# Kernel optimization log

Measured on AMD Instinct MI355X. Metric: run time of the kernel, lower is better.

Reference implementation:

```python
import jax, jax.numpy as jnp
import numpy as np


def setup_inputs() -> dict:
    key = jax.random.key(0)
    k = jax.random.split(key, 6)
    B = 65536
    x = jax.random.normal(k[0], (B, 784), dtype=jnp.float32)
    conv_w = jax.random.normal(k[1], (3, 3), dtype=jnp.float32)
    # torch Linear: weight [out,in], bias [out]; uniform(-1/sqrt(in),1/sqrt(in)) init approximated
    fc1_w = jax.random.uniform(k[2], (128, 26 * 26), dtype=jnp.float32, minval=-1, maxval=1) / jnp.sqrt(676.0)
    fc1_b = jax.random.uniform(k[3], (128,), dtype=jnp.float32, minval=-1, maxval=1) / jnp.sqrt(676.0)
    fc2_w = jax.random.uniform(k[4], (10, 128), dtype=jnp.float32, minval=-1, maxval=1) / jnp.sqrt(128.0)
    fc2_b = jax.random.uniform(k[5], (10,), dtype=jnp.float32, minval=-1, maxval=1) / jnp.sqrt(128.0)
    return {"x": x, "conv_w": conv_w, "fc1_w": fc1_w, "fc1_b": fc1_b, "fc2_w": fc2_w, "fc2_b": fc2_b}


def _forward(x, conv_w, fc1_w, fc1_b, fc2_w, fc2_b):
    B = x.shape[0]
    img = x.reshape(B, 1, 28, 28)  # NCHW, single channel
    kern = conv_w.reshape(1, 1, 3, 3)  # OIHW
    # valid 3x3 cross-correlation -> (B,1,26,26), same math as the nested-loop Convolve
    conv = jax.lax.conv_general_dilated(
        img, kern, window_strides=(1, 1), padding="VALID",
        dimension_numbers=("NCHW", "OIHW", "NCHW"))
    h = conv.reshape(B, 26 * 26)
    h = jax.nn.relu(h @ fc1_w.T + fc1_b)
    return h @ fc2_w.T + fc2_b  # (B,10)


def reference(x, conv_w, fc1_w, fc1_b, fc2_w, fc2_b):
    return _forward(x, conv_w, fc1_w, fc1_b, fc2_w, fc2_b)
```

## Files before the change

### kernel.cpp

```cpp
#include <hip/hip_runtime.h>
#include <hip/hip_bf16.h>

typedef float  f32x4  __attribute__((ext_vector_type(4)));
typedef short  short8 __attribute__((ext_vector_type(8)));

#define NKT 25
#define BM  128
#define AB  8192
#define BB  8192
#define BOFF (3 * AB)
#define POOLB (3 * AB + 4 * BB)

static __device__ __forceinline__ unsigned short f2bf(float f) {
    unsigned int u = __float_as_uint(f);
    unsigned int r = (u + 0x7fffu + ((u >> 16) & 1u)) >> 16;
    return (unsigned short)r;
}
static __device__ __forceinline__ float bf2f(unsigned short h) {
    return __uint_as_float(((unsigned int)h) << 16);
}
static __device__ __forceinline__ uint2 pack4(f32x4 v) {
    __hip_bfloat162 p0 = __float22bfloat162_rn(make_float2(v[0], v[1]));
    __hip_bfloat162 p1 = __float22bfloat162_rn(make_float2(v[2], v[3]));
    uint2 r;
    r.x = *reinterpret_cast<unsigned int*>(&p0);
    r.y = *reinterpret_cast<unsigned int*>(&p1);
    return r;
}

__global__ __launch_bounds__(256) void weff_prep(
    const float* __restrict__ fc1_w,
    const float* __restrict__ conv_w,
    unsigned short* __restrict__ weff4)
{
    int idx = blockIdx.x * 256 + threadIdx.x;
    if (idx >= 128 * 800) return;
    int o = idx / 800, p = idx - o * 800;
    float s = 0.f;
    if (p < 784) {
        int y = p / 28, xx = p - y * 28;
        #pragma unroll
        for (int dr = 0; dr < 3; ++dr) {
            int r = y - dr;
            if (r < 0 || r > 25) continue;
            #pragma unroll
            for (int dc = 0; dc < 3; ++dc) {
                int c = xx - dc;
                if (c < 0 || c > 25) continue;
                s += fc1_w[o * 676 + r * 26 + c] * conv_w[dr * 3 + dc];
            }
        }
    }
    int kt = p >> 5, kk = p & 31;
    weff4[kt * 4096 + (kk >> 3) * 1024 + o * 8 + (kk & 7)] = f2bf(s);
}

__global__ __launch_bounds__(512, 4) void fused_fwd(
    const float* __restrict__ x,
    const unsigned short* __restrict__ weff4,
    const float* __restrict__ fc1_b,
    const float* __restrict__ fc2_w,
    const float* __restrict__ fc2_b,
    float* __restrict__ out,
    int B)
{
    __shared__ __align__(16) char pool[POOLB];
    __shared__ float fc2w_s[1280];
    __shared__ float fc2b_s[16];

    const int tid  = threadIdx.x;
    const int lane = tid & 63;
    const int wid  = tid >> 6;
    const int wr   = wid >> 1;
    const int wc   = wid & 1;
    const int r16  = lane & 15;
    const int kc   = lane >> 4;
    const int m0   = blockIdx.x * BM;

    for (int i = tid; i < 1280; i += 512) fc2w_s[i] = fc2_w[i];
    if (tid < 10) fc2b_s[tid] = fc2_b[tid];
    asm volatile("s_waitcnt vmcnt(0)" ::: "memory");

    const int sr   = tid >> 3;
    const int g    = tid & 7;
    const int k2w  = g >> 1, half = g & 1;
    int row0 = m0 + sr;      if (row0 >= B) row0 = B - 1;
    int row1 = m0 + sr + 64; if (row1 >= B) row1 = B - 1;
    const float* xr0 = x + (size_t)row0 * 784;
    const float* xr1 = x + (size_t)row1 * 784;
    const int awb = k2w * 2048 + sr * 16 + half * 8;

    f32x4 av[3][2];

#define LD_A(s_, kt_) do {                                                    \
        int k_ = (kt_) * 32 + g * 4; if (k_ > 780) k_ = 0;                    \
        av[s_][0] = *reinterpret_cast<const f32x4*>(xr0 + k_);                \
        av[s_][1] = *reinterpret_cast<const f32x4*>(xr1 + k_);                \
    } while (0)

#define WR_A(s_, bi_) do {                                                    \
        uint2 q0_ = pack4(av[s_][0]);                                         \
        uint2 q1_ = pack4(av[s_][1]);                                         \
        char* ba_ = pool + (bi_) * AB + awb;                                  \
        *reinterpret_cast<uint2*>(ba_)        = q0_;                          \
        *reinterpret_cast<uint2*>(ba_ + 1024) = q1_;                          \
    } while (0)

#define GL_B(bi_, kt_) __builtin_amdgcn_global_load_lds(                      \
        (const __attribute__((address_space(1))) void*)                      \
            (weff4 + (size_t)(kt_) * 4096 + tid * 8),                         \
        (__attribute__((address_space(3))) void*)                            \
            (pool + BOFF + (bi_) * BB + tid * 16), 16, 0, 0)

    const int aoff = kc * 2048 + (wr * 32 + r16) * 16;
    const int boff = BOFF + kc * 2048 + (wc * 64 + r16) * 16;

    f32x4 acc[2][4];
    #pragma unroll
    for (int m = 0; m < 2; ++m)
        #pragma unroll
        for (int j = 0; j < 4; ++j) acc[m][j] = (f32x4)(0.f);

    LD_A(0, 0);
    GL_B(0, 0); GL_B(1, 1); GL_B(2, 2);
    LD_A(1, 1); LD_A(2, 2);
    WR_A(0, 0);

    #pragma unroll
    for (int i = 0; i < NKT; ++i) {
        asm volatile("s_waitcnt vmcnt(6) lgkmcnt(0)" ::: "memory");
        __builtin_amdgcn_s_barrier();
        __builtin_amdgcn_sched_barrier(0);

        const char* pa = pool + (i % 3) * AB;
        const char* pb = pool + (i % 4) * BB;
        short8 a0 = *reinterpret_cast<const short8*>(pa + aoff);
        short8 a1 = *reinterpret_cast<const short8*>(pa + aoff + 256);
        short8 b0 = *reinterpret_cast<const short8*>(pb + boff);
        short8 b1 = *reinterpret_cast<const short8*>(pb + boff + 256);
        short8 b2 = *reinterpret_cast<const short8*>(pb + boff + 512);
        short8 b3 = *reinterpret_cast<const short8*>(pb + boff + 768);

        const int kn = (i + 3 <= 24) ? (i + 3) : 24;
        LD_A((i + 3) % 3, kn);
        GL_B((i + 3) % 4, kn);
        WR_A((i + 1) % 3, (i + 1) % 3);

        acc[0][0] = __builtin_amdgcn_mfma_f32_16x16x32_bf16(a0, b0, acc[0][0], 0, 0, 0);
        acc[0][1] = __builtin_amdgcn_mfma_f32_16x16x32_bf16(a0, b1, acc[0][1], 0, 0, 0);
        acc[0][2] = __builtin_amdgcn_mfma_f32_16x16x32_bf16(a0, b2, acc[0][2], 0, 0, 0);
        acc[0][3] = __builtin_amdgcn_mfma_f32_16x16x32_bf16(a0, b3, acc[0][3], 0, 0, 0);
        acc[1][0] = __builtin_amdgcn_mfma_f32_16x16x32_bf16(a1, b0, acc[1][0], 0, 0, 0);
        acc[1][1] = __builtin_amdgcn_mfma_f32_16x16x32_bf16(a1, b1, acc[1][1], 0, 0, 0);
        acc[1][2] = __builtin_amdgcn_mfma_f32_16x16x32_bf16(a1, b2, acc[1][2], 0, 0, 0);
        acc[1][3] = __builtin_amdgcn_mfma_f32_16x16x32_bf16(a1, b3, acc[1][3], 0, 0, 0);
    }
#undef LD_A
#undef WR_A
#undef GL_B

    asm volatile("s_waitcnt vmcnt(0) lgkmcnt(0)" ::: "memory");
    __builtin_amdgcn_s_barrier();
    __builtin_amdgcn_sched_barrier(0);

    unsigned short (*Hs)[136] = (unsigned short (*)[136])pool;
    #pragma unroll
    for (int m = 0; m < 2; ++m) {
        #pragma unroll
        for (int j = 0; j < 4; ++j) {
            int ncol = wc * 64 + j * 16 + r16;
            float bias = fc1_b[ncol];
            #pragma unroll
            for (int r = 0; r < 4; ++r) {
                int mrow = wr * 32 + m * 16 + kc * 4 + r;
                float h = acc[m][j][r] + bias;
                Hs[mrow][ncol] = f2bf(h > 0.f ? h : 0.f);
            }
        }
    }
    __syncthreads();

    #pragma unroll
    for (int it = 0; it < 3; ++it) {
        int idx = it * 512 + tid;
        if (idx < BM * 10) {
            int row = idx / 10, j = idx - row * 10;
            if ((m0 + row) < B) {
                float sum = fc2b_s[j];
                const float* wrow = &fc2w_s[j * 128];
                #pragma unroll
                for (int n8 = 0; n8 < 16; ++n8) {
                    short8 h = *reinterpret_cast<const short8*>(&Hs[row][n8 * 8]);
                    #pragma unroll
                    for (int k2 = 0; k2 < 8; ++k2)
                        sum += bf2f(((unsigned short*)&h)[k2]) * wrow[n8 * 8 + k2];
                }
                out[(size_t)(m0 + row) * 10 + j] = sum;
            }
        }
    }
}

extern "C" void kernel_launch(void* const* d_in, const int* in_sizes, int n_in,
                              void* d_out, int out_size, void* d_ws, size_t ws_size,
                              hipStream_t stream) {
    const float* x      = (const float*)d_in[0];
    const float* conv_w = (const float*)d_in[1];
    const float* fc1_w  = (const float*)d_in[2];
    const float* fc1_b  = (const float*)d_in[3];
    const float* fc2_w  = (const float*)d_in[4];
    const float* fc2_b  = (const float*)d_in[5];
    float* out = (float*)d_out;
    unsigned short* weff4 = (unsigned short*)d_ws;

    int B = in_sizes[0] / 784;

    weff_prep<<<(128 * 800 + 255) / 256, 256, 0, stream>>>(fc1_w, conv_w, weff4);

    int nblk = (B + BM - 1) / BM;
    fused_fwd<<<nblk, 512, 0, stream>>>(x, weff4, fc1_b, fc2_w, fc2_b, out, B);
}
```

Measured before the change: 59.74 us.

## Halve row tile to 64, shrink LDS ring, move fc2 weights to bf16 global

Cuts the per-block M tile from 128 to 64 rows. Each wave now issues four MFMAs per k-step instead of eight, and the LDS B ring drops from four stages to three, so the launch bound rises to 8 blocks per CU. fc2 weights are converted to bf16 once in the prep kernel and read from global/L1 instead of being staged into LDS, which frees shared memory. The aim is higher occupancy to hide streaming latency on the x reads. In exchange, the weff B tiles are reloaded twice as often per row, and fc2 weights lose precision.

```diff
diff --git a/kernel.cpp b/kernel.cpp
--- a/kernel.cpp
+++ b/kernel.cpp
@@ -4,12 +4,12 @@
 typedef float  f32x4  __attribute__((ext_vector_type(4)));
 typedef short  short8 __attribute__((ext_vector_type(8)));
 
-#define NKT 25
-#define BM  128
-#define AB  8192
-#define BB  8192
-#define BOFF (3 * AB)
-#define POOLB (3 * AB + 4 * BB)
+#define NKT   25
+#define BM    64
+#define AB    4096
+#define BB    8192
+#define BOFFS (3 * AB)
+#define POOLB (3 * AB + 3 * BB)
 
 static __device__ __forceinline__ unsigned short f2bf(float f) {
     unsigned int u = __float_as_uint(f);
@@ -31,10 +31,12 @@
 __global__ __launch_bounds__(256) void weff_prep(
     const float* __restrict__ fc1_w,
     const float* __restrict__ conv_w,
-    unsigned short* __restrict__ weff4)
+    const float* __restrict__ fc2_w,
+    unsigned short* __restrict__ ws)
 {
     int idx = blockIdx.x * 256 + threadIdx.x;
     if (idx >= 128 * 800) return;
+    if (idx < 1280) ws[102400 + idx] = f2bf(fc2_w[idx]);
     int o = idx / 800, p = idx - o * 800;
     float s = 0.f;
     if (p < 784) {
@@ -52,21 +54,18 @@
         }
     }
     int kt = p >> 5, kk = p & 31;
-    weff4[kt * 4096 + (kk >> 3) * 1024 + o * 8 + (kk & 7)] = f2bf(s);
-}
-
-__global__ __launch_bounds__(512, 4) void fused_fwd(
+    ws[kt * 4096 + (kk >> 3) * 1024 + o * 8 + (kk & 7)] = f2bf(s);
+}
+
+__global__ __launch_bounds__(512, 8) void fused_fwd(
     const float* __restrict__ x,
     const unsigned short* __restrict__ weff4,
     const float* __restrict__ fc1_b,
-    const float* __restrict__ fc2_w,
     const float* __restrict__ fc2_b,
     float* __restrict__ out,
     int B)
 {
     __shared__ __align__(16) char pool[POOLB];
-    __shared__ float fc2w_s[1280];
-    __shared__ float fc2b_s[16];
 
     const int tid  = threadIdx.x;
     const int lane = tid & 63;
@@ -76,84 +75,69 @@
     const int r16  = lane & 15;
     const int kc   = lane >> 4;
     const int m0   = blockIdx.x * BM;
-
-    for (int i = tid; i < 1280; i += 512) fc2w_s[i] = fc2_w[i];
-    if (tid < 10) fc2b_s[tid] = fc2_b[tid];
-    asm volatile("s_waitcnt vmcnt(0)" ::: "memory");
-
-    const int sr   = tid >> 3;
-    const int g    = tid & 7;
-    const int k2w  = g >> 1, half = g & 1;
-    int row0 = m0 + sr;      if (row0 >= B) row0 = B - 1;
-    int row1 = m0 + sr + 64; if (row1 >= B) row1 = B - 1;
-    const float* xr0 = x + (size_t)row0 * 784;
-    const float* xr1 = x + (size_t)row1 * 784;
-    const int awb = k2w * 2048 + sr * 16 + half * 8;
-
-    f32x4 av[3][2];
+    const unsigned short* fc2wb = weff4 + 102400;
+
+    const int sr = tid >> 3;
+    const int g  = tid & 7;
+    int grow = m0 + sr; if (grow >= B) grow = B - 1;
+    const float* xr = x + (size_t)grow * 784;
+    const int awb = (g >> 1) * 1024 + sr * 16 + (g & 1) * 8;
+
+    f32x4 av[4];
 
 #define LD_A(s_, kt_) do {                                                    \
         int k_ = (kt_) * 32 + g * 4; if (k_ > 780) k_ = 0;                    \
-        av[s_][0] = *reinterpret_cast<const f32x4*>(xr0 + k_);                \
-        av[s_][1] = *reinterpret_cast<const f32x4*>(xr1 + k_);                \
+        av[s_] = *reinterpret_cast<const f32x4*>(xr + k_);                    \
     } while (0)
 
 #define WR_A(s_, bi_) do {                                                    \
-        uint2 q0_ = pack4(av[s_][0]);                                         \
-        uint2 q1_ = pack4(av[s_][1]);                                         \
-        char* ba_ = pool + (bi_) * AB + awb;                                  \
-        *reinterpret_cast<uint2*>(ba_)        = q0_;                          \
-        *reinterpret_cast<uint2*>(ba_ + 1024) = q1_;                          \
+        uint2 q_ = pack4(av[s_]);                                             \
+        *reinterpret_cast<uint2*>(pool + (bi_) * AB + awb) = q_;              \
     } while (0)
 
 #define GL_B(bi_, kt_) __builtin_amdgcn_global_load_lds(                      \
         (const __attribute__((address_space(1))) void*)                      \
             (weff4 + (size_t)(kt_) * 4096 + tid * 8),                         \
         (__attribute__((address_space(3))) void*)                            \
-            (pool + BOFF + (bi_) * BB + tid * 16), 16, 0, 0)
-
-    const int aoff = kc * 2048 + (wr * 32 + r16) * 16;
-    const int boff = BOFF + kc * 2048 + (wc * 64 + r16) * 16;
-
-    f32x4 acc[2][4];
-    #pragma unroll
-    for (int m = 0; m < 2; ++m)
-        #pragma unroll
-        for (int j = 0; j < 4; ++j) acc[m][j] = (f32x4)(0.f);
-
-    LD_A(0, 0);
-    GL_B(0, 0); GL_B(1, 1); GL_B(2, 2);
-    LD_A(1, 1); LD_A(2, 2);
+            (pool + BOFFS + (bi_) * BB + tid * 16), 16, 0, 0)
+
+    const int aoff = kc * 1024 + (wr * 16 + r16) * 16;
+    const int boff = BOFFS + kc * 2048 + (wc * 64 + r16) * 16;
+
+    f32x4 acc[4];
+    #pragma unroll
+    for (int j = 0; j < 4; ++j) acc[j] = (f32x4)(0.f);
+
+    asm volatile("s_waitcnt vmcnt(0)" ::: "memory");
+
+    GL_B(0, 0); GL_B(1, 1);
+    LD_A(0, 0); LD_A(1, 1); LD_A(2, 2);
     WR_A(0, 0);
 
     #pragma unroll
     for (int i = 0; i < NKT; ++i) {
-        asm volatile("s_waitcnt vmcnt(6) lgkmcnt(0)" ::: "memory");
+        asm volatile("s_waitcnt vmcnt(3) lgkmcnt(0)" ::: "memory");
         __builtin_amdgcn_s_barrier();
         __builtin_amdgcn_sched_barrier(0);
 
         const char* pa = pool + (i % 3) * AB;
-        const char* pb = pool + (i % 4) * BB;
+        const char* pb = pool + (i % 3) * BB;
         short8 a0 = *reinterpret_cast<const short8*>(pa + aoff);
-        short8 a1 = *reinterpret_cast<const short8*>(pa + aoff + 256);
         short8 b0 = *reinterpret_cast<const short8*>(pb + boff);
         short8 b1 = *reinterpret_cast<const short8*>(pb + boff + 256);
         short8 b2 = *reinterpret_cast<const short8*>(pb + boff + 512);
         short8 b3 = *reinterpret_cast<const short8*>(pb + boff + 768);
 
-        const int kn = (i + 3 <= 24) ? (i + 3) : 24;
-        LD_A((i + 3) % 3, kn);
-        GL_B((i + 3) % 4, kn);
-        WR_A((i + 1) % 3, (i + 1) % 3);
-
-        acc[0][0] = __builtin_amdgcn_mfma_f32_16x16x32_bf16(a0, b0, acc[0][0], 0, 0, 0);
-        acc[0][1] = __builtin_amdgcn_mfma_f32_16x16x32_bf16(a0, b1, acc[0][1], 0, 0, 0);
-        acc[0][2] = __builtin_amdgcn_mfma_f32_16x16x32_bf16(a0, b2, acc[0][2], 0, 0, 0);
-        acc[0][3] = __builtin_amdgcn_mfma_f32_16x16x32_bf16(a0, b3, acc[0][3], 0, 0, 0);
-        acc[1][0] = __builtin_amdgcn_mfma_f32_16x16x32_bf16(a1, b0, acc[1][0], 0, 0, 0);
-        acc[1][1] = __builtin_amdgcn_mfma_f32_16x16x32_bf16(a1, b1, acc[1][1], 0, 0, 0);
-        acc[1][2] = __builtin_amdgcn_mfma_f32_16x16x32_bf16(a1, b2, acc[1][2], 0, 0, 0);
-        acc[1][3] = __builtin_amdgcn_mfma_f32_16x16x32_bf16(a1, b3, acc[1][3], 0, 0, 0);
+        const int kb = (i + 2 <= 24) ? (i + 2) : 24;
+        const int ka = (i + 3 <= 24) ? (i + 3) : 24;
+        GL_B((i + 2) % 3, kb);
+        LD_A((i + 3) % 4, ka);
+        WR_A((i + 1) % 4, (i + 1) % 3);
+
+        acc[0] = __builtin_amdgcn_mfma_f32_16x16x32_bf16(a0, b0, acc[0], 0, 0, 0);
+        acc[1] = __builtin_amdgcn_mfma_f32_16x16x32_bf16(a0, b1, acc[1], 0, 0, 0);
+        acc[2] = __builtin_amdgcn_mfma_f32_16x16x32_bf16(a0, b2, acc[2], 0, 0, 0);
+        acc[3] = __builtin_amdgcn_mfma_f32_16x16x32_bf16(a0, b3, acc[3], 0, 0, 0);
     }
 #undef LD_A
 #undef WR_A
@@ -165,35 +149,34 @@
 
     unsigned short (*Hs)[136] = (unsigned short (*)[136])pool;
     #pragma unroll
-    for (int m = 0; m < 2; ++m) {
+    for (int j = 0; j < 4; ++j) {
+        int ncol = wc * 64 + j * 16 + r16;
+        float bias = fc1_b[ncol];
         #pragma unroll
-        for (int j = 0; j < 4; ++j) {
-            int ncol = wc * 64 + j * 16 + r16;
-            float bias = fc1_b[ncol];
-            #pragma unroll
-            for (int r = 0; r < 4; ++r) {
-                int mrow = wr * 32 + m * 16 + kc * 4 + r;
-                float h = acc[m][j][r] + bias;
-                Hs[mrow][ncol] = f2bf(h > 0.f ? h : 0.f);
-            }
+        for (int r = 0; r < 4; ++r) {
+            int mrow = wr * 16 + kc * 4 + r;
+            float h = acc[j][r] + bias;
+            Hs[mrow][ncol] = f2bf(h > 0.f ? h : 0.f);
         }
     }
     __syncthreads();
 
     #pragma unroll
-    for (int it = 0; it < 3; ++it) {
+    for (int it = 0; it < 2; ++it) {
         int idx = it * 512 + tid;
         if (idx < BM * 10) {
             int row = idx / 10, j = idx - row * 10;
             if ((m0 + row) < B) {
-                float sum = fc2b_s[j];
-                const float* wrow = &fc2w_s[j * 128];
+                float sum = fc2_b[j];
+                const unsigned short* wrow = fc2wb + j * 128;
                 #pragma unroll
                 for (int n8 = 0; n8 < 16; ++n8) {
                     short8 h = *reinterpret_cast<const short8*>(&Hs[row][n8 * 8]);
+                    short8 w = *reinterpret_cast<const short8*>(wrow + n8 * 8);
                     #pragma unroll
                     for (int k2 = 0; k2 < 8; ++k2)
-                        sum += bf2f(((unsigned short*)&h)[k2]) * wrow[n8 * 8 + k2];
+                        sum += bf2f(((unsigned short*)&h)[k2]) *
+                               bf2f(((unsigned short*)&w)[k2]);
                 }
                 out[(size_t)(m0 + row) * 10 + j] = sum;
             }
@@ -211,12 +194,12 @@
     const float* fc2_w  = (const float*)d_in[4];
     const float* fc2_b  = (const float*)d_in[5];
     float* out = (float*)d_out;
-    unsigned short* weff4 = (unsigned short*)d_ws;
+    unsigned short* ws = (unsigned short*)d_ws;
 
     int B = in_sizes[0] / 784;
 
-    weff_prep<<<(128 * 800 + 255) / 256, 256, 0, stream>>>(fc1_w, conv_w, weff4);
+    weff_prep<<<(128 * 800 + 255) / 256, 256, 0, stream>>>(fc1_w, conv_w, fc2_w, ws);
 
     int nblk = (B + BM - 1) / BM;
-    fused_fwd<<<nblk, 512, 0, stream>>>(x, weff4, fc1_b, fc2_w, fc2_b, out, B);
-}
+    fused_fwd<<<nblk, 512, 0, stream>>>(x, ws, fc1_b, fc2_b, out, B);
+}
```

Measured after the change: 58.71 us (median of 2 runs). Within noise of the previous version (-1.7%).
